# Kernel optimization log

Hardware: AMD Instinct MI355X
Metric: run time of the kernel (lower is better)

## Reference

```python
import jax, jax.numpy as jnp
import numpy as np

B, N, QD, ED, H, DH = 2, 512, 512, 11, 4, 64
INNER = H * DH
SCALE = DH ** -0.5


def setup_inputs() -> dict:
    key = jax.random.key(0)
    ks = jax.random.split(key, 16)
    s = 0.02
    x = jax.random.normal(ks[0], (B, N, QD), jnp.float32)
    mask = jax.random.randint(ks[1], (B, N, N), 0, 2).astype(bool)
    mask = mask | jnp.eye(N, dtype=bool)[None]  # ensure each row attends somewhere
    edge_attr = jax.random.normal(ks[2], (B, N, N, ED), jnp.float32)
    return {
        "x": x,
        "adjacency_mask": mask,
        "edge_attr": edge_attr,
        "Wq": jax.random.normal(ks[3], (QD, INNER), jnp.float32) * s,
        "Wk": jax.random.normal(ks[4], (QD, INNER), jnp.float32) * s,
        "Wv": jax.random.normal(ks[5], (QD, INNER), jnp.float32) * s,
        "Web1": jax.random.normal(ks[6], (ED, INNER), jnp.float32) * s,
        "beb1": jnp.zeros((INNER,), jnp.float32),
        "Web2": jax.random.normal(ks[7], (INNER, H), jnp.float32) * s,
        "beb2": jnp.zeros((H,), jnp.float32),
        "Wev1": jax.random.normal(ks[8], (ED, INNER), jnp.float32) * s,
        "bev1": jnp.zeros((INNER,), jnp.float32),
        "Wev2": jax.random.normal(ks[9], (INNER, INNER), jnp.float32) * s,
        "bev2": jnp.zeros((INNER,), jnp.float32),
        "Wo": jax.random.normal(ks[10], (INNER, QD), jnp.float32) * s,
        "bo": jnp.zeros((QD,), jnp.float32),
    }


def reference(x, adjacency_mask, edge_attr, Wq, Wk, Wv, Web1, beb1, Web2, beb2,
              Wev1, bev1, Wev2, bev2, Wo, bo):
    b, n, _ = x.shape
    # project and split heads: b n (h d) -> b h n d
    def heads(t):
        return t.reshape(b, n, H, DH).transpose(0, 2, 1, 3)
    q = heads(x @ Wq)
    k = heads(x @ Wk)
    v = heads(x @ Wv)

    # edge bias MLP: [b,i,j,ed] -> [b,i,j,h] -> [b,h,i,j]  (exact GELU, matching torch default)
    eb_h = jax.nn.gelu(edge_attr @ Web1 + beb1, approximate=False)
    edge_bias = (eb_h @ Web2 + beb2).transpose(0, 3, 1, 2)
    # edge value MLP: [b,i,j,ed] -> [b,i,j,inner] -> [b,h,i,j,d]
    ev_h = jax.nn.gelu(edge_attr @ Wev1 + bev1, approximate=False)
    edge_value = (ev_h @ Wev2 + bev2).reshape(b, n, n, H, DH).transpose(0, 3, 1, 2, 4)

    sim = jnp.einsum('bhid,bhjd->bhij', q, k) * SCALE + edge_bias
    neg = -jnp.finfo(sim.dtype).max
    sim = jnp.where(adjacency_mask[:, None, :, :], sim, neg)
    attn = jax.nn.softmax(sim, axis=-1)

    # out = sum_j attn * (v_j + edge_value_ij) = attn@v + einsum over edge_value
    out = jnp.einsum('bhij,bhjd->bhid', attn, v) \
        + jnp.einsum('bhij,bhijd->bhid', attn, edge_value)
    out = out.transpose(0, 2, 1, 3).reshape(b, n, INNER)
    return out @ Wo + bo, attn
```

## Files before the change

kernel.cpp:

```cpp
#include <hip/hip_runtime.h>
#include <hip/hip_bf16.h>
#include <math.h>

#define NB 2
#define NN 512
#define QD 512
#define ED 11
#define NH 4
#define DH 64
#define INNER 256
#define SCALE 0.125f
#define NEGMAX -3.402823466e38f

typedef const __hip_bfloat16* bfp;
typedef float f32x2 __attribute__((ext_vector_type(2)));
typedef __attribute__((ext_vector_type(4))) float f32x4;
typedef __attribute__((ext_vector_type(4))) short s16x4;

template<int FM>
__device__ __forceinline__ float ldf(const void* p, size_t i) {
    if (FM) return ((const float*)p)[i];
    return __bfloat162float(((bfp)p)[i]);
}

__device__ __forceinline__ unsigned short f2bf(float x) {
    __hip_bfloat16 h = __float2bfloat16(x);
    return __builtin_bit_cast(unsigned short, h);
}

template<int FM>
__device__ __forceinline__ unsigned short ldb(const void* p, size_t i) {
    if (FM) return f2bf(((const float*)p)[i]);
    return ((const unsigned short*)p)[i];
}

__device__ __forceinline__ f32x4 mfma16(s16x4 a, s16x4 b, f32x4 c) {
    return __builtin_amdgcn_mfma_f32_16x16x16bf16_1k(a, b, c, 0, 0, 0);
}

#define QKV_F   (NB*NN*768)
#define OIN_F   (NB*NN*INNER)
#define OFF_QKV   0
#define OFF_OIN   (OFF_QKV + QKV_F)
#define OFF_FLAGS (OFF_OIN + OIN_F)
#define OFF_KBF   (OFF_FLAGS + 4)

__device__ __forceinline__ f32x2 pkfma(f32x2 a, f32x2 b, f32x2 c) {
    return __builtin_elementwise_fma(a, b, c);
}
__device__ __forceinline__ f32x2 mk2(float x, float y) { f32x2 r; r.x = x; r.y = y; return r; }
__device__ __forceinline__ f32x2 bc2(float x) { f32x2 r; r.x = x; r.y = x; return r; }
__device__ __forceinline__ f32x4 bc4(float x) { f32x4 r; r.x = x; r.y = x; r.z = x; r.w = x; return r; }

__device__ __forceinline__ f32x2 gelu2(f32x2 x) {
    f32x2 t = x * x;
    f32x2 p = pkfma(t, bc2(-0.0023746715f), bc2(0.019947114f));
    p = pkfma(t, p, bc2(-0.13298076f));
    p = pkfma(t, p, bc2(0.7978845608f));
    return x * pkfma(bc2(0.5f) * x, p, bc2(0.5f));
}

__device__ __forceinline__ s16x4 gelu_pack(f32x4 d) {
    f32x2 glo = gelu2(mk2(d.x, d.y));
    f32x2 ghi = gelu2(mk2(d.z, d.w));
    s16x4 b;
    b.x = (short)f2bf(glo.x); b.y = (short)f2bf(glo.y);
    b.z = (short)f2bf(ghi.x); b.w = (short)f2bf(ghi.y);
    return b;
}

__device__ __forceinline__ bool maskAt(int mode, const void* p, size_t idx) {
    switch (mode) {
        case 0:  return ((const int*)p)[idx] != 0;
        case 1:  return ((const unsigned char*)p)[idx] != 0;
        case 2:  return ((const unsigned short*)p)[idx] != 0;
        default: return ((const float*)p)[idx] != 0.0f;
    }
}

__global__ void detect_modes(const void* x, const void* mask, int* flags) {
    __shared__ int sh_f32, sh_i32ok, sh_u8ok;
    if (threadIdx.x == 0) { sh_f32 = 0; sh_i32ok = 1; sh_u8ok = 1; }
    __syncthreads();
    const unsigned short* hx = (const unsigned short*)x;
    int f32hit = 0;
    for (int i = threadIdx.x; i < 4096; i += 256) {
        unsigned e = (hx[i] >> 7) & 0xFFu;
        if (e >= 0xC0u) f32hit = 1;
    }
    if (f32hit) atomicOr(&sh_f32, 1);
    const unsigned int* pm = (const unsigned int*)mask;
    int bad_i = 0, bad_b = 0;
    for (int i = threadIdx.x; i < 1024; i += 256) {
        unsigned v = pm[i];
        if (v > 1u) bad_i = 1;
        if ((v & 255u) > 1u || ((v >> 8) & 255u) > 1u ||
            ((v >> 16) & 255u) > 1u || ((v >> 24) & 255u) > 1u) bad_b = 1;
    }
    if (bad_i) atomicAnd(&sh_i32ok, 0);
    if (bad_b) atomicAnd(&sh_u8ok, 0);
    __syncthreads();
    if (threadIdx.x == 0) {
        flags[0] = sh_f32;
        int mm;
        if (sh_i32ok) mm = 0;
        else if (sh_u8ok) mm = 1;
        else mm = (((const unsigned short*)mask)[0] != 0) ? 2 : 3;
        flags[1] = mm;
    }
}

template<int FM>
__global__ __launch_bounds__(1024) void qkv_kernel(
        const void* x, const void* Wq, const void* Wk, const void* Wv,
        const int* flags, float* qkv, unsigned short* kbf) {
    if (flags[0] != FM) return;
    __shared__ float xs[4][QD];
    __shared__ float pl[4][4][3][256];
    const int r0 = blockIdx.x * 4;
    const int t = threadIdx.x;
    const int qq = t >> 8;
    const int c  = t & 255;
    for (int idx = t; idx < 4 * QD; idx += 1024) {
        int r = idx >> 9, cc = idx & (QD - 1);
        xs[r][cc] = ldf<FM>(x, (size_t)(r0 + r) * QD + cc);
    }
    __syncthreads();
    float acc[4][3];
#pragma unroll
    for (int r = 0; r < 4; r++) { acc[r][0] = 0.f; acc[r][1] = 0.f; acc[r][2] = 0.f; }
    const int k0 = qq * 128, k1 = k0 + 128;
    for (int k = k0; k < k1; k++) {
        float wq = ldf<FM>(Wq, (size_t)k * INNER + c);
        float wk = ldf<FM>(Wk, (size_t)k * INNER + c);
        float wv = ldf<FM>(Wv, (size_t)k * INNER + c);
#pragma unroll
        for (int r = 0; r < 4; r++) {
            float xv = xs[r][k];
            acc[r][0] = fmaf(xv, wq, acc[r][0]);
            acc[r][1] = fmaf(xv, wk, acc[r][1]);
            acc[r][2] = fmaf(xv, wv, acc[r][2]);
        }
    }
#pragma unroll
    for (int r = 0; r < 4; r++) {
#pragma unroll
        for (int m = 0; m < 3; m++) pl[qq][r][m][c] = acc[r][m];
    }
    __syncthreads();
    if (t < 256) {
#pragma unroll
        for (int r = 0; r < 4; r++) {
            size_t base = (size_t)(r0 + r) * 768;
#pragma unroll
            for (int m = 0; m < 3; m++) {
                float s = pl[0][r][m][t] + pl[1][r][m][t]
                        + pl[2][r][m][t] + pl[3][r][m][t];
                qkv[base + m * 256 + t] = s;
                if (m == 1) kbf[(size_t)(r0 + r) * 256 + t] = f2bf(s);
            }
        }
    }
}

#define SM_EA    0
#define SM_W1T   20480
#define SM_WV1T  30720
#define SM_W2T   40960
#define SM_QST   43072
#define SM_JLIST 45184
#define SM_CTL   46208
#define SM_SIMT  46272
#define SM_TOTAL 54464

template<int FM>
__global__ __launch_bounds__(512, 4) void attn_ev_kernel(
        const void* ea, const void* mask,
        const void* Web1, const void* beb1, const void* Web2, const void* beb2,
        const void* Wev1, const void* bev1, const void* Wev2, const void* bev2,
        const int* flags, const float* qkv, const unsigned short* kbf,
        float* oin, void* d_out) {
    if (flags[0] != FM) return;
    const int mmode = flags[1];
    __shared__ __align__(16) char smem_raw[SM_TOTAL];
    unsigned short* ea_s  = (unsigned short*)(smem_raw + SM_EA);
    unsigned short* w1t   = (unsigned short*)(smem_raw + SM_W1T);
    unsigned short* wv1t  = (unsigned short*)(smem_raw + SM_WV1T);
    unsigned short* w2t   = (unsigned short*)(smem_raw + SM_W2T);
    unsigned short* qst   = (unsigned short*)(smem_raw + SM_QST);
    unsigned short* jlist = (unsigned short*)(smem_raw + SM_JLIST);
    int* ctl              = (int*)(smem_raw + SM_CTL);
    float* simT           = (float*)(smem_raw + SM_SIMT);

    const int blk = blockIdx.x;
    const int b = blk >> 9, i = blk & (NN - 1);
    const int t = threadIdx.x;
    const int lane = t & 63, wave = t >> 6;
    const int lj = lane & 15;
    const int g  = lane >> 4;
    const f32x4 FZ = {0.f, 0.f, 0.f, 0.f};
    const size_t mrow = (size_t)(b * NN + i) * NN;

    {
        const size_t ea_row = (size_t)(b * NN + i) * (NN * ED);
        for (int idx = t; idx < NN * 16; idx += 512) {
            int j = idx >> 4, k = idx & 15;
            unsigned short v;
            if (k < ED)       v = ldb<FM>(ea, ea_row + j * ED + k);
            else if (k == ED) v = 0x3F80;
            else              v = 0;
            ea_s[j * 20 + k] = v;
        }
        for (int idx = t; idx < 256 * 16; idx += 512) {
            int c = idx >> 4, k = idx & 15;
            unsigned short v1 = 0, v2 = 0;
            if (k < ED) { v1 = ldb<FM>(Web1, (size_t)k * INNER + c);
                          v2 = ldb<FM>(Wev1, (size_t)k * INNER + c); }
            else if (k == ED) { v1 = ldb<FM>(beb1, c); v2 = ldb<FM>(bev1, c); }
            w1t[c * 20 + k]  = v1;
            wv1t[c * 20 + k] = v2;
        }
        const float* qrow = qkv + (size_t)(b * NN + i) * 768;
        for (int idx = t; idx < 4 * 256; idx += 512) {
            int h = idx >> 8, c = idx & 255;
            w2t[h * 264 + c] = ldb<FM>(Web2, (size_t)c * NH + h);
            qst[h * 264 + c] = ((c >> 6) == h) ? f2bf(qrow[c] * SCALE) : (unsigned short)0;
        }
        {
            float4 nf; nf.x = NEGMAX; nf.y = NEGMAX; nf.z = NEGMAX; nf.w = NEGMAX;
            *(float4*)&simT[t * 4] = nf;
        }
    }
    const bool um = maskAt(mmode, mask, mrow + t);
    const unsigned long long bal = __ballot(um);
    if (lane == 0) {
        ctl[wave] = __popcll(bal);
        unsigned long long nb = ~bal;
        ctl[8 + wave] = nb ? (wave * 64 + (int)__ffsll((long long)nb) - 1) : 0x7fffffff;
    }
    __syncthreads();

    int M, padJ;
    {
        int s = 0, mybase = 0, pj = 0x7fffffff;
#pragma unroll
        for (int w = 0; w < 8; w++) {
            if (w == wave) mybase = s;
            s += ctl[w];
            pj = min(pj, ctl[8 + w]);
        }
        M = s;
        padJ = (pj == 0x7fffffff) ? 0 : pj;
        if (um) jlist[mybase + __popcll(bal & ((1ull << lane) - 1ull))] = (unsigned short)t;
    }
    __syncthreads();
    const int T = (M + 15) >> 4;

    {
        float bb2v[4];
#pragma unroll
        for (int h = 0; h < 4; h++) bb2v[h] = ldf<FM>(beb2, h);
        const unsigned short* a2base = w2t + (lj & 3) * 264;
        const unsigned short* a3base = qst + (lj & 3) * 264;
        for (int tt = wave; tt < T; tt += 8) {
            const int sbase = tt * 16;
            const int slot = sbase + lj;
            const int jme = (slot < M) ? (int)jlist[slot] : padJ;
            const unsigned short* kbase = kbf + ((size_t)(b * NN) + jme) * 256;
            s16x4 kf0[8], kf1[8];
#pragma unroll
            for (int u = 0; u < 8; u++) kf0[u] = *(const s16x4*)&kbase[u * 16 + 4 * g];
            const s16x4 b1 = *(const s16x4*)&ea_s[jme * 20 + 4 * g];
            f32x4 accA = FZ;
#pragma unroll
            for (int hb = 0; hb < 2; hb++) {
                if (hb == 1) {
#pragma unroll
                    for (int u = 0; u < 8; u++)
                        kf1[u] = *(const s16x4*)&kbase[(8 + u) * 16 + 4 * g];
                }
                f32x4 d1s[8];
#pragma unroll
                for (int u = 0; u < 8; u++) {
                    s16x4 wa1 = *(const s16x4*)&w1t[((hb * 8 + u) * 16 + lj) * 20 + 4 * g];
                    d1s[u] = mfma16(wa1, b1, FZ);
                }
                __builtin_amdgcn_sched_barrier(0);
                s16x4 b2s[8];
#pragma unroll
                for (int u = 0; u < 8; u++) b2s[u] = gelu_pack(d1s[u]);
                __builtin_amdgcn_sched_barrier(0);
#pragma unroll
                for (int u = 0; u < 8; u++) {
                    s16x4 wa2 = *(const s16x4*)&a2base[(hb * 8 + u) * 16 + 4 * g];
                    accA = mfma16(wa2, b2s[u], accA);
                }
                __builtin_amdgcn_sched_barrier(0);
            }
            f32x4 accB0 = FZ, accB1 = FZ;
#pragma unroll
            for (int ct = 0; ct < 16; ct++) {
                s16x4 a3 = *(const s16x4*)&a3base[ct * 16 + 4 * g];
                s16x4 kv = (ct < 8) ? kf0[ct] : kf1[ct - 8];
                if (ct & 1) accB1 = mfma16(a3, kv, accB1);
                else        accB0 = mfma16(a3, kv, accB0);
            }
            if (lane < 16) {
                const int sl2 = sbase + lane;
                if (sl2 < M) {
                    const int j = (int)jlist[sl2];
                    float4 sv;
                    sv.x = accA.x + accB0.x + accB1.x + bb2v[0];
                    sv.y = accA.y + accB0.y + accB1.y + bb2v[1];
                    sv.z = accA.z + accB0.z + accB1.z + bb2v[2];
                    sv.w = accA.w + accB0.w + accB1.w + bb2v[3];
                    *(float4*)&simT[j * 4] = sv;
                }
            }
        }
    }
    __syncthreads();

    if (wave < NH) {
        const int h = wave;
        float sv[8], pv[8];
        float mx = NEGMAX;
#pragma unroll
        for (int it = 0; it < 8; it++) {
            sv[it] = simT[(lane + it * 64) * 4 + h];
            mx = fmaxf(mx, sv[it]);
        }
#pragma unroll
        for (int off = 1; off < 64; off <<= 1) mx = fmaxf(mx, __shfl_xor(mx, off, 64));
        float sum = 0.f;
#pragma unroll
        for (int it = 0; it < 8; it++) { pv[it] = __expf(sv[it] - mx); sum += pv[it]; }
#pragma unroll
        for (int off = 1; off < 64; off <<= 1) sum += __shfl_xor(sum, off, 64);
        float inv = 1.0f / sum;
        size_t base = (size_t)NB * NN * QD + ((size_t)(b * NH + h) * NN + i) * NN;
#pragma unroll
        for (int it = 0; it < 8; it++) {
            float a = pv[it] * inv;
            simT[(lane + it * 64) * 4 + h] = a;
            if (FM) ((float*)d_out)[base + lane + it * 64] = a;
            else    ((__hip_bfloat16*)d_out)[base + lane + it * 64] = __float2bfloat16(a);
        }
    }
    __syncthreads();

    f32x4 awacc[4];
#pragma unroll
    for (int cc = 0; cc < 4; cc++) awacc[cc] = FZ;
    f32x4 avp4 = FZ;
    const int jhalf = wave >> 2, cq = wave & 3;
    {
        s16x4 b1r[4];
#pragma unroll
        for (int cc = 0; cc < 4; cc++)
            b1r[cc] = *(const s16x4*)&wv1t[((cq * 4 + cc) * 16 + lj) * 20 + 4 * g];
        const int h4 = lj & 3;
        for (int tt = jhalf; tt < T; tt += 2) {
            const int sbase = tt * 16;
            const int slotm = sbase + lj;
            const int jm = (slotm < M) ? (int)jlist[slotm] : padJ;
            const s16x4 a1 = *(const s16x4*)&ea_s[jm * 20 + 4 * g];
            s16x4 a2;
            {
                const int s0 = sbase + 4 * g;
                const int ja = (s0 + 0 < M) ? (int)jlist[s0 + 0] : padJ;
                const int jb = (s0 + 1 < M) ? (int)jlist[s0 + 1] : padJ;
                const int jc = (s0 + 2 < M) ? (int)jlist[s0 + 2] : padJ;
                const int jd = (s0 + 3 < M) ? (int)jlist[s0 + 3] : padJ;
                a2.x = (short)f2bf(simT[ja * 4 + h4]);
                a2.y = (short)f2bf(simT[jb * 4 + h4]);
                a2.z = (short)f2bf(simT[jc * 4 + h4]);
                a2.w = (short)f2bf(simT[jd * 4 + h4]);
            }
            f32x4 d1s[4];
#pragma unroll
            for (int cc = 0; cc < 4; cc++) d1s[cc] = mfma16(a1, b1r[cc], FZ);
            __builtin_amdgcn_sched_barrier(0);
            s16x4 b2s[4];
#pragma unroll
            for (int cc = 0; cc < 4; cc++) b2s[cc] = gelu_pack(d1s[cc]);
            __builtin_amdgcn_sched_barrier(0);
#pragma unroll
            for (int cc = 0; cc < 4; cc++)
                awacc[cc] = mfma16(a2, b2s[cc], awacc[cc]);
            __builtin_amdgcn_sched_barrier(0);
        }
        const float* vrow0 = qkv + (size_t)(b * NN) * 768 + 512;
        const int Mw = ((M + 63) & ~63) >> 3;
        const int s0w = wave * Mw;
        for (int sb = 0; sb < Mw; sb += 8) {
            float at8[8]; f32x4 vv[8];
#pragma unroll
            for (int u = 0; u < 8; u++) {
                const int slot = s0w + sb + u;
                const int j = (slot < M) ? (int)jlist[slot] : padJ;
                at8[u] = simT[j * 4 + g];
                vv[u] = *(const f32x4*)(vrow0 + (size_t)j * 768 + 4 * lane);
            }
#pragma unroll
            for (int u = 0; u < 8; u++)
                avp4 = __builtin_elementwise_fma(bc4(at8[u]), vv[u], avp4);
        }
    }
    __syncthreads();

    {
        float* pbufAW = (float*)smem_raw;
        float* pbufAV = (float*)smem_raw + 2048;
        if (lane < 16) {
#pragma unroll
            for (int cc = 0; cc < 4; cc++) {
                const int cbase = (cq * 4 + cc) * 16 + lane;
                pbufAW[jhalf * 1024 + 0 * 256 + cbase] = awacc[cc].x;
                pbufAW[jhalf * 1024 + 1 * 256 + cbase] = awacc[cc].y;
                pbufAW[jhalf * 1024 + 2 * 256 + cbase] = awacc[cc].z;
                pbufAW[jhalf * 1024 + 3 * 256 + cbase] = awacc[cc].w;
            }
        }
        *(float4*)&pbufAV[wave * 256 + 4 * lane] = *(float4*)&avp4;
        __syncthreads();
        float* accw = (float*)(smem_raw + SM_SIMT);
        for (int idx = t; idx < 1280; idx += 512) {
            if (idx < 1024) {
                accw[idx] = pbufAW[idx] + pbufAW[1024 + idx];
            } else {
                const int c = idx - 1024;
                float s = 0.f;
#pragma unroll
                for (int w = 0; w < 8; w++) s += pbufAV[w * 256 + c];
                accw[idx] = s;
            }
        }
    }
    __syncthreads();

    {
        const float* accw = (const float*)(smem_raw + SM_SIMT);
        float* pepi = (float*)(smem_raw + SM_SIMT) + 1280;
        const int c = t & 255;
        const int hh = c >> 6;
        const int half = t >> 8;
        float o = 0.f;
        const int cp0 = half * 128, cp1 = cp0 + 128;
        for (int cp = cp0; cp < cp1; cp += 4) {
            const float4 aw4 = *(const float4*)&accw[hh * 256 + cp];
            o = fmaf(aw4.x, ldf<FM>(Wev2, (size_t)(cp + 0) * INNER + c), o);
            o = fmaf(aw4.y, ldf<FM>(Wev2, (size_t)(cp + 1) * INNER + c), o);
            o = fmaf(aw4.z, ldf<FM>(Wev2, (size_t)(cp + 2) * INNER + c), o);
            o = fmaf(aw4.w, ldf<FM>(Wev2, (size_t)(cp + 3) * INNER + c), o);
        }
        pepi[t] = o;
        __syncthreads();
        if (t < 256) {
            float out_v = ldf<FM>(bev2, c) + accw[1024 + c] + pepi[c] + pepi[c + 256];
            oin[(size_t)(b * NN + i) * INNER + c] = out_v;
        }
    }
}

template<int FM>
__global__ __launch_bounds__(1024) void outproj_kernel(
        const float* oin, const void* Wo, const void* bo,
        const int* flags, void* d_out) {
    if (flags[0] != FM) return;
    __shared__ float os[4][INNER];
    __shared__ float pp[2][4][QD];
    const int r0 = blockIdx.x * 4;
    const int t = threadIdx.x;
    const int qq = t >> 9;
    const int co = t & 511;
    for (int idx = t; idx < 4 * INNER; idx += 1024) {
        os[idx >> 8][idx & 255] = oin[(size_t)(r0 + (idx >> 8)) * INNER + (idx & 255)];
    }
    __syncthreads();
    float acc[4] = {0.f, 0.f, 0.f, 0.f};
    const int k0 = qq * 128, k1 = k0 + 128;
    for (int k = k0; k < k1; k++) {
        float w = ldf<FM>(Wo, (size_t)k * QD + co);
#pragma unroll
        for (int r = 0; r < 4; r++) acc[r] = fmaf(os[r][k], w, acc[r]);
    }
#pragma unroll
    for (int r = 0; r < 4; r++) pp[qq][r][co] = acc[r];
    __syncthreads();
    if (t < 512) {
        float bv = ldf<FM>(bo, t);
#pragma unroll
        for (int r = 0; r < 4; r++) {
            float s = pp[0][r][t] + pp[1][r][t] + bv;
            size_t i0 = (size_t)(r0 + r) * QD + t;
            if (FM) ((float*)d_out)[i0] = s;
            else    ((__hip_bfloat16*)d_out)[i0] = __float2bfloat16(s);
        }
    }
}

extern "C" void kernel_launch(void* const* d_in, const int* in_sizes, int n_in,
                              void* d_out, int out_size, void* d_ws, size_t ws_size,
                              hipStream_t stream) {
    (void)in_sizes; (void)n_in; (void)out_size; (void)ws_size;
    const void* x    = d_in[0];
    const void* mask = d_in[1];
    const void* ea   = d_in[2];
    const void* Wq   = d_in[3];
    const void* Wk   = d_in[4];
    const void* Wv   = d_in[5];
    const void* Web1 = d_in[6];
    const void* beb1 = d_in[7];
    const void* Web2 = d_in[8];
    const void* beb2 = d_in[9];
    const void* Wev1 = d_in[10];
    const void* bev1 = d_in[11];
    const void* Wev2 = d_in[12];
    const void* bev2 = d_in[13];
    const void* Wo   = d_in[14];
    const void* bo   = d_in[15];

    float* ws    = (float*)d_ws;
    float* qkv   = ws + OFF_QKV;
    float* oin   = ws + OFF_OIN;
    int*   flags = (int*)(ws + OFF_FLAGS);
    unsigned short* kbf = (unsigned short*)(ws + OFF_KBF);

    detect_modes<<<1, 256, 0, stream>>>(x, mask, flags);

    qkv_kernel<0><<<NB * NN / 4, 1024, 0, stream>>>(x, Wq, Wk, Wv, flags, qkv, kbf);
    qkv_kernel<1><<<NB * NN / 4, 1024, 0, stream>>>(x, Wq, Wk, Wv, flags, qkv, kbf);

    attn_ev_kernel<0><<<NB * NN, 512, 0, stream>>>(ea, mask, Web1, beb1, Web2, beb2,
                                                   Wev1, bev1, Wev2, bev2,
                                                   flags, qkv, kbf, oin, d_out);
    attn_ev_kernel<1><<<NB * NN, 512, 0, stream>>>(ea, mask, Web1, beb1, Web2, beb2,
                                                   Wev1, bev1, Wev2, bev2,
                                                   flags, qkv, kbf, oin, d_out);

    outproj_kernel<0><<<NB * NN / 4, 1024, 0, stream>>>(oin, Wo, bo, flags, d_out);
    outproj_kernel<1><<<NB * NN / 4, 1024, 0, stream>>>(oin, Wo, bo, flags, d_out);
}
```

Baseline: 222.6 us.

## Move QKV and output projections to bf16 MFMA with pre-packed weights

Replaces the scalar FP32 FMA QKV and output projection kernels with bf16 16x16x16 MFMA kernels. A new pack kernel runs every call and converts Wq/Wk/Wv/Wo into a k-interleaved bf16 layout so each lane loads four consecutive-k weights with one vector load. Activations are staged in LDS as bf16. This lowers the compute cost of the projection GEMMs at the price of an extra launch, a weight repack pass, and reduced precision on the fp32 input path.

```diff
diff --git a/kernel.cpp b/kernel.cpp
--- a/kernel.cpp
+++ b/kernel.cpp
@@ -44,6 +44,8 @@
 #define OFF_OIN   (OFF_QKV + QKV_F)
 #define OFF_FLAGS (OFF_OIN + OIN_F)
 #define OFF_KBF   (OFF_FLAGS + 4)
+#define OFF_WPK   (OFF_KBF + 131072)
+#define OFF_WOPK  (OFF_WPK + 196608)
 
 __device__ __forceinline__ f32x2 pkfma(f32x2 a, f32x2 b, f32x2 c) {
     return __builtin_elementwise_fma(a, b, c);
@@ -111,55 +113,97 @@
 }
 
 template<int FM>
-__global__ __launch_bounds__(1024) void qkv_kernel(
-        const void* x, const void* Wq, const void* Wk, const void* Wv,
-        const int* flags, float* qkv, unsigned short* kbf) {
+__global__ __launch_bounds__(256) void pack_w_kernel(
+        const void* Wq, const void* Wk, const void* Wv, const void* Wo,
+        const int* flags, unsigned short* wpk, unsigned short* wopk) {
     if (flags[0] != FM) return;
-    __shared__ float xs[4][QD];
-    __shared__ float pl[4][4][3][256];
-    const int r0 = blockIdx.x * 4;
+    const int id = blockIdx.x * 256 + threadIdx.x;
+    if (id < 98304) {
+        const int c = id % 768, a = id / 768;
+        const void* W = (c < 256) ? Wq : ((c < 512) ? Wk : Wv);
+        const int cc = c & 255;
+        unsigned short* dst = wpk + ((size_t)a * 768 + c) * 4;
+#pragma unroll
+        for (int e = 0; e < 4; e++)
+            dst[e] = ldb<FM>(W, (size_t)(4 * a + e) * INNER + cc);
+    } else {
+        const int id2 = id - 98304;
+        const int c = id2 % 512, a = id2 / 512;
+        unsigned short* dst = wopk + ((size_t)a * 512 + c) * 4;
+#pragma unroll
+        for (int e = 0; e < 4; e++)
+            dst[e] = ldb<FM>(Wo, (size_t)(4 * a + e) * QD + c);
+    }
+}
+
+template<int FM>
+__global__ __launch_bounds__(256) void qkv_mfma_kernel(
+        const void* x, const int* flags, const unsigned short* wpk,
+        float* qkv, unsigned short* kbf) {
+    if (flags[0] != FM) return;
+    __shared__ unsigned short xs[16 * 520];
+    const int rb  = blockIdx.x / 12;
+    const int cgq = blockIdx.x % 12;
+    const int r0 = rb * 16;
     const int t = threadIdx.x;
-    const int qq = t >> 8;
-    const int c  = t & 255;
-    for (int idx = t; idx < 4 * QD; idx += 1024) {
-        int r = idx >> 9, cc = idx & (QD - 1);
-        xs[r][cc] = ldf<FM>(x, (size_t)(r0 + r) * QD + cc);
-    }
-    __syncthreads();
-    float acc[4][3];
-#pragma unroll
-    for (int r = 0; r < 4; r++) { acc[r][0] = 0.f; acc[r][1] = 0.f; acc[r][2] = 0.f; }
-    const int k0 = qq * 128, k1 = k0 + 128;
-    for (int k = k0; k < k1; k++) {
-        float wq = ldf<FM>(Wq, (size_t)k * INNER + c);
-        float wk = ldf<FM>(Wk, (size_t)k * INNER + c);
-        float wv = ldf<FM>(Wv, (size_t)k * INNER + c);
-#pragma unroll
-        for (int r = 0; r < 4; r++) {
-            float xv = xs[r][k];
-            acc[r][0] = fmaf(xv, wq, acc[r][0]);
-            acc[r][1] = fmaf(xv, wk, acc[r][1]);
-            acc[r][2] = fmaf(xv, wv, acc[r][2]);
-        }
-    }
-#pragma unroll
-    for (int r = 0; r < 4; r++) {
-#pragma unroll
-        for (int m = 0; m < 3; m++) pl[qq][r][m][c] = acc[r][m];
-    }
-    __syncthreads();
-    if (t < 256) {
-#pragma unroll
-        for (int r = 0; r < 4; r++) {
-            size_t base = (size_t)(r0 + r) * 768;
-#pragma unroll
-            for (int m = 0; m < 3; m++) {
-                float s = pl[0][r][m][t] + pl[1][r][m][t]
-                        + pl[2][r][m][t] + pl[3][r][m][t];
-                qkv[base + m * 256 + t] = s;
-                if (m == 1) kbf[(size_t)(r0 + r) * 256 + t] = f2bf(s);
-            }
-        }
+    const int lane = t & 63, wave = t >> 6;
+    const int lj = lane & 15, g = lane >> 4;
+    for (int idx = t; idx < 16 * 512; idx += 256) {
+        int r = idx >> 9, c = idx & 511;
+        xs[r * 520 + c] = ldb<FM>(x, (size_t)(r0 + r) * QD + c);
+    }
+    __syncthreads();
+    const int cb = cgq * 64 + wave * 16;
+    f32x4 acc = {0.f, 0.f, 0.f, 0.f};
+#pragma unroll 8
+    for (int ks = 0; ks < 32; ks++) {
+        s16x4 a = *(const s16x4*)&xs[lj * 520 + ks * 16 + 4 * g];
+        s16x4 b = *(const s16x4*)&wpk[((size_t)(ks * 4 + g) * 768 + cb + lj) * 4];
+        acc = mfma16(a, b, acc);
+    }
+    const int col = cb + lj;
+#pragma unroll
+    for (int e = 0; e < 4; e++) {
+        const int row = r0 + 4 * g + e;
+        float v = acc[e];
+        qkv[(size_t)row * 768 + col] = v;
+        if (col >= 256 && col < 512) kbf[(size_t)row * 256 + (col - 256)] = f2bf(v);
+    }
+}
+
+template<int FM>
+__global__ __launch_bounds__(256) void outproj_mfma_kernel(
+        const float* oin, const unsigned short* wopk, const void* bo,
+        const int* flags, void* d_out) {
+    if (flags[0] != FM) return;
+    __shared__ unsigned short os[16 * 264];
+    const int rb  = blockIdx.x >> 3;
+    const int cgq = blockIdx.x & 7;
+    const int r0 = rb * 16;
+    const int t = threadIdx.x;
+    const int lane = t & 63, wave = t >> 6;
+    const int lj = lane & 15, g = lane >> 4;
+    for (int idx = t; idx < 16 * 256; idx += 256) {
+        int r = idx >> 8, c = idx & 255;
+        os[r * 264 + c] = f2bf(oin[(size_t)(r0 + r) * INNER + c]);
+    }
+    __syncthreads();
+    const int cb = cgq * 64 + wave * 16;
+    f32x4 acc = {0.f, 0.f, 0.f, 0.f};
+#pragma unroll
+    for (int ks = 0; ks < 16; ks++) {
+        s16x4 a = *(const s16x4*)&os[lj * 264 + ks * 16 + 4 * g];
+        s16x4 b = *(const s16x4*)&wopk[((size_t)(ks * 4 + g) * 512 + cb + lj) * 4];
+        acc = mfma16(a, b, acc);
+    }
+    const int col = cb + lj;
+    const float bv = ldf<FM>(bo, col);
+#pragma unroll
+    for (int e = 0; e < 4; e++) {
+        const int row = r0 + 4 * g + e;
+        float v = acc[e] + bv;
+        if (FM) ((float*)d_out)[(size_t)row * QD + col] = v;
+        else    ((__hip_bfloat16*)d_out)[(size_t)row * QD + col] = __float2bfloat16(v);
     }
 }
 
@@ -459,43 +503,6 @@
         if (t < 256) {
             float out_v = ldf<FM>(bev2, c) + accw[1024 + c] + pepi[c] + pepi[c + 256];
             oin[(size_t)(b * NN + i) * INNER + c] = out_v;
-        }
-    }
-}
-
-template<int FM>
-__global__ __launch_bounds__(1024) void outproj_kernel(
-        const float* oin, const void* Wo, const void* bo,
-        const int* flags, void* d_out) {
-    if (flags[0] != FM) return;
-    __shared__ float os[4][INNER];
-    __shared__ float pp[2][4][QD];
-    const int r0 = blockIdx.x * 4;
-    const int t = threadIdx.x;
-    const int qq = t >> 9;
-    const int co = t & 511;
-    for (int idx = t; idx < 4 * INNER; idx += 1024) {
-        os[idx >> 8][idx & 255] = oin[(size_t)(r0 + (idx >> 8)) * INNER + (idx & 255)];
-    }
-    __syncthreads();
-    float acc[4] = {0.f, 0.f, 0.f, 0.f};
-    const int k0 = qq * 128, k1 = k0 + 128;
-    for (int k = k0; k < k1; k++) {
-        float w = ldf<FM>(Wo, (size_t)k * QD + co);
-#pragma unroll
-        for (int r = 0; r < 4; r++) acc[r] = fmaf(os[r][k], w, acc[r]);
-    }
-#pragma unroll
-    for (int r = 0; r < 4; r++) pp[qq][r][co] = acc[r];
-    __syncthreads();
-    if (t < 512) {
-        float bv = ldf<FM>(bo, t);
-#pragma unroll
-        for (int r = 0; r < 4; r++) {
-            float s = pp[0][r][t] + pp[1][r][t] + bv;
-            size_t i0 = (size_t)(r0 + r) * QD + t;
-            if (FM) ((float*)d_out)[i0] = s;
-            else    ((__hip_bfloat16*)d_out)[i0] = __float2bfloat16(s);
         }
     }
 }
@@ -525,12 +532,17 @@
     float* qkv   = ws + OFF_QKV;
     float* oin   = ws + OFF_OIN;
     int*   flags = (int*)(ws + OFF_FLAGS);
-    unsigned short* kbf = (unsigned short*)(ws + OFF_KBF);
+    unsigned short* kbf  = (unsigned short*)(ws + OFF_KBF);
+    unsigned short* wpk  = (unsigned short*)(ws + OFF_WPK);
+    unsigned short* wopk = (unsigned short*)(ws + OFF_WOPK);
 
     detect_modes<<<1, 256, 0, stream>>>(x, mask, flags);
 
-    qkv_kernel<0><<<NB * NN / 4, 1024, 0, stream>>>(x, Wq, Wk, Wv, flags, qkv, kbf);
-    qkv_kernel<1><<<NB * NN / 4, 1024, 0, stream>>>(x, Wq, Wk, Wv, flags, qkv, kbf);
+    pack_w_kernel<0><<<512, 256, 0, stream>>>(Wq, Wk, Wv, Wo, flags, wpk, wopk);
+    pack_w_kernel<1><<<512, 256, 0, stream>>>(Wq, Wk, Wv, Wo, flags, wpk, wopk);
+
+    qkv_mfma_kernel<0><<<768, 256, 0, stream>>>(x, flags, wpk, qkv, kbf);
+    qkv_mfma_kernel<1><<<768, 256, 0, stream>>>(x, flags, wpk, qkv, kbf);
 
     attn_ev_kernel<0><<<NB * NN, 512, 0, stream>>>(ea, mask, Web1, beb1, Web2, beb2,
                                                    Wev1, bev1, Wev2, bev2,
@@ -539,6 +551,6 @@
                                                    Wev1, bev1, Wev2, bev2,
                                                    flags, qkv, kbf, oin, d_out);
 
-    outproj_kernel<0><<<NB * NN / 4, 1024, 0, stream>>>(oin, Wo, bo, flags, d_out);
-    outproj_kernel<1><<<NB * NN / 4, 1024, 0, stream>>>(oin, Wo, bo, flags, d_out);
-}
+    outproj_mfma_kernel<0><<<512, 256, 0, stream>>>(oin, wopk, bo, flags, d_out);
+    outproj_mfma_kernel<1><<<512, 256, 0, stream>>>(oin, wopk, bo, flags, d_out);
+}
```

Result: faster. 216.7 us (-2.7%).
